# Kernel tuning notes

Measured on AMD Instinct MI355X. Metric: run time of the kernel, lower is better.

The kernel has to match this reference:

```python
import jax, jax.numpy as jnp
import numpy as np
import math

HIDDEN = 1024
HEADS = 16
HEAD_DIM = HIDDEN // HEADS
B, S = 4, 2048


def setup_inputs() -> dict:
    key = jax.random.key(0)
    ks = jax.random.split(key, 9)
    std = 1.0 / math.sqrt(HIDDEN)
    return {
        "query": jax.random.normal(ks[0], (B, S, HIDDEN), jnp.float32),
        "key": jax.random.normal(ks[1], (B, S, HIDDEN), jnp.float32),
        "value": jax.random.normal(ks[2], (B, S, HIDDEN), jnp.float32),
        "q_w": jax.random.normal(ks[3], (HIDDEN, HIDDEN), jnp.float32) * std,
        "q_b": jax.random.normal(ks[4], (HIDDEN,), jnp.float32) * 0.02,
        "k_w": jax.random.normal(ks[5], (HIDDEN, HIDDEN), jnp.float32) * std,
        "k_b": jax.random.normal(ks[6], (HIDDEN,), jnp.float32) * 0.02,
        "v_w": jax.random.normal(ks[7], (HIDDEN, HIDDEN), jnp.float32) * std,
        "v_b": jax.random.normal(ks[8], (HIDDEN,), jnp.float32) * 0.02,
    }


def _split_heads(x):
    # [B, S, H] -> [B, heads, S, head_dim]
    b, s, _ = x.shape
    return x.reshape(b, s, HEADS, HEAD_DIM).transpose(0, 2, 1, 3)


def reference(query, key, value, q_w, q_b, k_w, k_b, v_w, v_b):
    # Linear projections (torch Linear: x @ W^T + b; here weights stored as [in, out])
    q = _split_heads(query @ q_w + q_b)   # [B, h, S, d]
    k = _split_heads(key @ k_w + k_b)
    v = _split_heads(value @ v_w + v_b)
    scale = 1.0 / math.sqrt(HEAD_DIM)
    scores = jnp.einsum("bhqd,bhkd->bhqk", q, k) * scale  # [B, h, S, S]
    # NOTE: faithful to source bug — context uses raw scaled scores, NOT softmax probs.
    # (softmax is computed in the original but its result is unused for the output.)
    ctx = jnp.einsum("bhqk,bhkd->bhqd", scores, v)
    ctx = ctx.transpose(0, 2, 1, 3).reshape(query.shape[0], query.shape[1], HIDDEN)
    return ctx
```

## Files before the change

kernel.cpp:

```cpp
#include <hip/hip_runtime.h>
#include <stdint.h>

#define HIDDEN 1024
#define HEADS 16
#define HEAD_DIM 64
#define BATCH 4
#define SEQ 2048
#define ROWS (BATCH * SEQ)

typedef float f32x4 __attribute__((ext_vector_type(4)));
typedef short bf16x8 __attribute__((ext_vector_type(8)));

__device__ __forceinline__ uint16_t f32_to_bf16_rne(float f) {
    uint32_t u = __float_as_uint(f);
    uint32_t r = u + 0x7FFFu + ((u >> 16) & 1u);
    return (uint16_t)(r >> 16);
}
__device__ __forceinline__ float bf16_to_f32(uint16_t u) {
    return __uint_as_float(((uint32_t)u) << 16);
}

__global__ __launch_bounds__(256) void cvt_kernel(const float* __restrict__ Xq,
                                                  const float* __restrict__ Xk,
                                                  const float* __restrict__ Xv,
                                                  uint16_t* __restrict__ Xb) {
    int z = blockIdx.x >> 11;
    const float* X = z == 0 ? Xq : (z == 1 ? Xk : Xv);
    uint16_t* out = Xb + (size_t)z * ROWS * HIDDEN;
    size_t base = (size_t)(blockIdx.x & 2047) * 1024 + threadIdx.x;
    const float4* Xi = (const float4*)X;
    float4 f0 = Xi[base];
    float4 f1 = Xi[base + 256];
    float4 f2 = Xi[base + 512];
    float4 f3 = Xi[base + 768];
    uint2* Oi = (uint2*)out;
    uint2 p;
    p.x = (uint32_t)f32_to_bf16_rne(f0.x) | ((uint32_t)f32_to_bf16_rne(f0.y) << 16);
    p.y = (uint32_t)f32_to_bf16_rne(f0.z) | ((uint32_t)f32_to_bf16_rne(f0.w) << 16);
    Oi[base] = p;
    p.x = (uint32_t)f32_to_bf16_rne(f1.x) | ((uint32_t)f32_to_bf16_rne(f1.y) << 16);
    p.y = (uint32_t)f32_to_bf16_rne(f1.z) | ((uint32_t)f32_to_bf16_rne(f1.w) << 16);
    Oi[base + 256] = p;
    p.x = (uint32_t)f32_to_bf16_rne(f2.x) | ((uint32_t)f32_to_bf16_rne(f2.y) << 16);
    p.y = (uint32_t)f32_to_bf16_rne(f2.z) | ((uint32_t)f32_to_bf16_rne(f2.w) << 16);
    Oi[base + 512] = p;
    p.x = (uint32_t)f32_to_bf16_rne(f3.x) | ((uint32_t)f32_to_bf16_rne(f3.y) << 16);
    p.y = (uint32_t)f32_to_bf16_rne(f3.z) | ((uint32_t)f32_to_bf16_rne(f3.w) << 16);
    Oi[base + 768] = p;
}

__global__ __launch_bounds__(256) void wt_kernel(const float* __restrict__ Wk,
                                                 const float* __restrict__ Wv,
                                                 uint16_t* __restrict__ Wt) {
    const float* W = blockIdx.z == 0 ? Wk : Wv;
    uint16_t* out = Wt + (size_t)blockIdx.z * HIDDEN * HIDDEN;
    __shared__ float tile[64][65];
    int k0 = blockIdx.x * 64, n0 = blockIdx.y * 64;
    int r = threadIdx.x >> 6, c = threadIdx.x & 63;
    for (int it = 0; it < 16; ++it) {
        int rr = r + 4 * it;
        tile[rr][c] = W[(size_t)(k0 + rr) * HIDDEN + n0 + c];
    }
    __syncthreads();
    for (int it = 0; it < 16; ++it) {
        int rr = r + 4 * it;
        out[(size_t)(n0 + rr) * HIDDEN + k0 + c] = f32_to_bf16_rne(tile[c][rr]);
    }
}

__global__ __launch_bounds__(256) void proj_gemm(const uint16_t* __restrict__ Xkv,
                                                 const uint16_t* __restrict__ Wt,
                                                 const float* __restrict__ Bk,
                                                 const float* __restrict__ Bv,
                                                 uint16_t* __restrict__ KV) {
    const int z = blockIdx.z;
    const uint16_t* X = Xkv + (size_t)z * ROWS * HIDDEN;
    const uint16_t* W = Wt + (size_t)z * HIDDEN * HIDDEN;
    const float* bias = z == 0 ? Bk : Bv;
    uint16_t* out = KV + (size_t)z * ROWS * HIDDEN;

    __shared__ uint16_t slds[16384];

    const int tid = threadIdx.x;
    const int lane = tid & 63;
    const int w = tid >> 6;
    const int wm = (w >> 1) * 64;
    const int wn = (w & 1) * 64;
    const int m_lane = lane & 15;
    const int kq = lane >> 4;
    const int m0 = blockIdx.x * 128;
    const int n0 = blockIdx.y * 128;

    f32x4 acc[4][4] = {};

    for (int kb = 0; kb < HIDDEN; kb += 64) {
        for (int t = 0; t < 4; ++t) {
            int gbase = (w * 4 + t) * 64;
            int g = gbase + lane;
            int r = g >> 3;
            int c = (g & 7) ^ (r & 7);
            const uint16_t* srcA = X + (size_t)(m0 + r) * HIDDEN + kb + c * 8;
            __builtin_amdgcn_global_load_lds(
                (const __attribute__((address_space(1))) uint32_t*)srcA,
                (__attribute__((address_space(3))) uint32_t*)(&slds[gbase * 8]),
                16, 0, 0);
            const uint16_t* srcB = W + (size_t)(n0 + r) * HIDDEN + kb + c * 8;
            __builtin_amdgcn_global_load_lds(
                (const __attribute__((address_space(1))) uint32_t*)srcB,
                (__attribute__((address_space(3))) uint32_t*)(&slds[8192 + gbase * 8]),
                16, 0, 0);
        }
        __syncthreads();
        for (int ks = 0; ks < 2; ++ks) {
            int cbase = ks * 4 + kq;
            bf16x8 af[4], bfr[4];
            for (int i = 0; i < 4; ++i) {
                int r = wm + i * 16 + m_lane;
                int p = cbase ^ (r & 7);
                af[i] = *(const bf16x8*)(&slds[r * 64 + p * 8]);
            }
            for (int j = 0; j < 4; ++j) {
                int nr = wn + j * 16 + m_lane;
                int p = cbase ^ (nr & 7);
                bfr[j] = *(const bf16x8*)(&slds[8192 + nr * 64 + p * 8]);
            }
            for (int i = 0; i < 4; ++i)
                for (int j = 0; j < 4; ++j)
                    acc[i][j] = __builtin_amdgcn_mfma_f32_16x16x32_bf16(
                        af[i], bfr[j], acc[i][j], 0, 0, 0);
        }
        __syncthreads();
    }

    for (int j = 0; j < 4; ++j) {
        int col = n0 + wn + j * 16 + m_lane;
        float bj = bias[col];
        for (int i = 0; i < 4; ++i) {
            int rbase = m0 + wm + i * 16 + kq * 4;
            for (int rg = 0; rg < 4; ++rg) {
                float v = acc[i][j][rg] + bj;
                out[(size_t)(rbase + rg) * HIDDEN + col] = f32_to_bf16_rne(v);
            }
        }
    }
}

__global__ __launch_bounds__(256) void kv_kernel(const uint16_t* __restrict__ KV,
                                                 float* __restrict__ P) {
    const uint16_t* K = KV;
    const uint16_t* V = KV + (size_t)ROWS * HIDDEN;
    const int bh = blockIdx.x;
    const int sc = blockIdx.y;
    const int b = bh >> 4, h = bh & 15;
    const int tid = threadIdx.x;
    const size_t base = ((size_t)b * SEQ + sc * 256) * HIDDEN + h * 64;

    __shared__ float kk[16][64];
    __shared__ float vv[16][64];
    float acc[4][4] = {};
    const int i0 = (tid >> 4) * 4, j0 = (tid & 15) * 4;

    for (int batch = 0; batch < 16; ++batch) {
        __syncthreads();
        {
            int t = tid & 127;
            int row = t >> 3, c = t & 7;
            const uint16_t* src =
                (tid < 128 ? K : V) + base + (size_t)(batch * 16 + row) * HIDDEN + c * 8;
            float* dst = (tid < 128 ? &kk[row][c * 8] : &vv[row][c * 8]);
            bf16x8 d = *(const bf16x8*)src;
            for (int e = 0; e < 8; ++e) dst[e] = bf16_to_f32((uint16_t)d[e]);
        }
        __syncthreads();
        for (int r = 0; r < 16; ++r) {
            f32x4 ka = *(const f32x4*)(&kk[r][i0]);
            f32x4 va = *(const f32x4*)(&vv[r][j0]);
            for (int a = 0; a < 4; ++a)
                for (int bb = 0; bb < 4; ++bb)
                    acc[a][bb] += ka[a] * va[bb];
        }
    }
    float* Pp = P + ((size_t)bh * 8 + sc) * 4096;
    for (int a = 0; a < 4; ++a) {
        f32x4 row;
        for (int bb = 0; bb < 4; ++bb) row[bb] = acc[a][bb] * 0.125f;
        *(f32x4*)(&Pp[(i0 + a) * 64 + j0]) = row;
    }
}

__global__ __launch_bounds__(256) void wprime_kernel(const float* __restrict__ Wq,
                                                     const float* __restrict__ bq,
                                                     const float* __restrict__ P,
                                                     uint16_t* __restrict__ Wpt,
                                                     float* __restrict__ bp) {
    const int h = blockIdx.x;
    const int r0 = blockIdx.y * 64;
    const int b = blockIdx.z;
    const int tid = threadIdx.x;

    __shared__ float Mh[64][65];
    __shared__ float Wl[64][65];
    const float* Pp = P + ((size_t)(b * 16 + h)) * 8 * 4096;
    for (int it = 0; it < 16; ++it) {
        int e = it * 256 + tid;
        int a = e >> 6, c = e & 63;
        float s = 0.f;
        for (int sc = 0; sc < 8; ++sc) s += Pp[sc * 4096 + e];
        Mh[a][c] = s;
        Wl[a][c] = Wq[(size_t)(r0 + a) * HIDDEN + h * 64 + c];
    }
    __syncthreads();

    const int r = tid & 63;
    const int jbase = tid >> 6;
    float acc[16] = {};
    for (int i = 0; i < 64; ++i) {
        float wv = Wl[r][i];
        for (int jj = 0; jj < 16; ++jj)
            acc[jj] += wv * Mh[i][jbase + 4 * jj];
    }
    uint16_t* Wb = Wpt + (size_t)b * HIDDEN * HIDDEN;
    for (int jj = 0; jj < 16; ++jj) {
        int n = h * 64 + jbase + 4 * jj;
        Wb[(size_t)n * HIDDEN + r0 + r] = f32_to_bf16_rne(acc[jj]);
    }

    if (blockIdx.y == 0 && tid < 64) {
        int j = tid;
        float s = 0.f;
        for (int i = 0; i < 64; ++i) s += bq[h * 64 + i] * Mh[i][j];
        bp[b * HIDDEN + h * 64 + j] = s;
    }
}

__global__ __launch_bounds__(256) void final_gemm(const uint16_t* __restrict__ Xq,
                                                  const uint16_t* __restrict__ Wpt,
                                                  const float* __restrict__ bp,
                                                  float* __restrict__ out) {
    __shared__ uint16_t slds[16384];

    const int tid = threadIdx.x;
    const int lane = tid & 63;
    const int w = tid >> 6;
    const int wm = (w >> 1) * 64;
    const int wn = (w & 1) * 64;
    const int m_lane = lane & 15;
    const int kq = lane >> 4;
    const int m0 = blockIdx.x * 128;
    const int n0 = blockIdx.y * 128;
    const int batch = m0 >> 11;
    const uint16_t* W = Wpt + (size_t)batch * HIDDEN * HIDDEN;
    const float* bias = bp + batch * HIDDEN;

    f32x4 acc[4][4] = {};

    for (int kb = 0; kb < HIDDEN; kb += 64) {
        for (int t = 0; t < 4; ++t) {
            int gbase = (w * 4 + t) * 64;
            int g = gbase + lane;
            int r = g >> 3;
            int c = (g & 7) ^ (r & 7);
            const uint16_t* srcA = Xq + (size_t)(m0 + r) * HIDDEN + kb + c * 8;
            __builtin_amdgcn_global_load_lds(
                (const __attribute__((address_space(1))) uint32_t*)srcA,
                (__attribute__((address_space(3))) uint32_t*)(&slds[gbase * 8]),
                16, 0, 0);
            const uint16_t* srcB = W + (size_t)(n0 + r) * HIDDEN + kb + c * 8;
            __builtin_amdgcn_global_load_lds(
                (const __attribute__((address_space(1))) uint32_t*)srcB,
                (__attribute__((address_space(3))) uint32_t*)(&slds[8192 + gbase * 8]),
                16, 0, 0);
        }
        __syncthreads();
        for (int ks = 0; ks < 2; ++ks) {
            int cbase = ks * 4 + kq;
            bf16x8 af[4], bfr[4];
            for (int i = 0; i < 4; ++i) {
                int r = wm + i * 16 + m_lane;
                int p = cbase ^ (r & 7);
                af[i] = *(const bf16x8*)(&slds[r * 64 + p * 8]);
            }
            for (int j = 0; j < 4; ++j) {
                int nr = wn + j * 16 + m_lane;
                int p = cbase ^ (nr & 7);
                bfr[j] = *(const bf16x8*)(&slds[8192 + nr * 64 + p * 8]);
            }
            for (int i = 0; i < 4; ++i)
                for (int j = 0; j < 4; ++j)
                    acc[i][j] = __builtin_amdgcn_mfma_f32_16x16x32_bf16(
                        af[i], bfr[j], acc[i][j], 0, 0, 0);
        }
        __syncthreads();
    }

    for (int j = 0; j < 4; ++j) {
        int col = n0 + wn + j * 16 + m_lane;
        float bj = bias[col];
        for (int i = 0; i < 4; ++i) {
            int rbase = m0 + wm + i * 16 + kq * 4;
            for (int rg = 0; rg < 4; ++rg)
                out[(size_t)(rbase + rg) * HIDDEN + col] = acc[i][j][rg] + bj;
        }
    }
}

extern "C" void kernel_launch(void* const* d_in, const int* in_sizes, int n_in,
                              void* d_out, int out_size, void* d_ws, size_t ws_size,
                              hipStream_t stream) {
    const float* Xq = (const float*)d_in[0];
    const float* Xk = (const float*)d_in[1];
    const float* Xv = (const float*)d_in[2];
    const float* Wq = (const float*)d_in[3];
    const float* Bq = (const float*)d_in[4];
    const float* Wk = (const float*)d_in[5];
    const float* Bk = (const float*)d_in[6];
    const float* Wv = (const float*)d_in[7];
    const float* Bv = (const float*)d_in[8];
    float* out = (float*)d_out;

    char* ws = (char*)d_ws;
    uint16_t* Xb = (uint16_t*)ws;
    uint16_t* KV = (uint16_t*)(ws + 50331648);
    uint16_t* Wt = (uint16_t*)(ws + 83886080);
    float* P = (float*)(ws + 88080384);
    uint16_t* Wpt = (uint16_t*)(ws + 96468992);
    float* bp = (float*)(ws + 104857600);

    cvt_kernel<<<dim3(3 * 2048), 256, 0, stream>>>(Xq, Xk, Xv, Xb);
    wt_kernel<<<dim3(16, 16, 2), 256, 0, stream>>>(Wk, Wv, Wt);

    const uint16_t* Xkv = Xb + (size_t)ROWS * HIDDEN;
    proj_gemm<<<dim3(64, 8, 2), 256, 0, stream>>>(Xkv, Wt, Bk, Bv, KV);
    kv_kernel<<<dim3(64, 8), 256, 0, stream>>>(KV, P);
    wprime_kernel<<<dim3(16, 16, 4), 256, 0, stream>>>(Wq, Bq, P, Wpt, bp);
    final_gemm<<<dim3(64, 8), 256, 0, stream>>>(Xb, Wpt, bp, out);
}
```

Baseline: 272.2 us.

## Reassociate K^T V via input Gram matrix instead of projecting K and V

Instead of projecting K and V over all 8192 rows and then forming per-head K^T V, this computes the per-batch Gram matrix Xv^T Xk (1024x1024 over 2048 tokens) and then multiplies it by the weights. Bias terms are added through row sums of the inputs and small matvec kernels. This removes the large projection GEMM but adds transposed bf16 conversions, an extra 1024^3-per-batch GEMM, atomics and several small kernels. Precision changes too, because the Gram matrix is stored in bf16.

```diff
diff --git a/kernel.cpp b/kernel.cpp
--- a/kernel.cpp
+++ b/kernel.cpp
@@ -20,20 +20,15 @@
     return __uint_as_float(((uint32_t)u) << 16);
 }
 
-__global__ __launch_bounds__(256) void cvt_kernel(const float* __restrict__ Xq,
-                                                  const float* __restrict__ Xk,
-                                                  const float* __restrict__ Xv,
-                                                  uint16_t* __restrict__ Xb) {
-    int z = blockIdx.x >> 11;
-    const float* X = z == 0 ? Xq : (z == 1 ? Xk : Xv);
-    uint16_t* out = Xb + (size_t)z * ROWS * HIDDEN;
-    size_t base = (size_t)(blockIdx.x & 2047) * 1024 + threadIdx.x;
-    const float4* Xi = (const float4*)X;
+__global__ __launch_bounds__(256) void cvt_q(const float* __restrict__ Xq,
+                                             uint16_t* __restrict__ XqB) {
+    size_t base = (size_t)blockIdx.x * 1024 + threadIdx.x;
+    const float4* Xi = (const float4*)Xq;
     float4 f0 = Xi[base];
     float4 f1 = Xi[base + 256];
     float4 f2 = Xi[base + 512];
     float4 f3 = Xi[base + 768];
-    uint2* Oi = (uint2*)out;
+    uint2* Oi = (uint2*)XqB;
     uint2 p;
     p.x = (uint32_t)f32_to_bf16_rne(f0.x) | ((uint32_t)f32_to_bf16_rne(f0.y) << 16);
     p.y = (uint32_t)f32_to_bf16_rne(f0.z) | ((uint32_t)f32_to_bf16_rne(f0.w) << 16);
@@ -49,6 +44,36 @@
     Oi[base + 768] = p;
 }
 
+__global__ __launch_bounds__(256) void cvt_t(const float* __restrict__ Xk,
+                                             const float* __restrict__ Xv,
+                                             uint16_t* __restrict__ XkT,
+                                             uint16_t* __restrict__ XvT,
+                                             float* __restrict__ rk,
+                                             float* __restrict__ rv) {
+    const int z = blockIdx.z >> 2, b = blockIdx.z & 3;
+    const float* X = z ? Xv : Xk;
+    uint16_t* XT = z ? XvT : XkT;
+    float* rsum = z ? rv : rk;
+    __shared__ float tile[64][65];
+    const int s0 = blockIdx.x * 64, i0 = blockIdx.y * 64;
+    const int r = threadIdx.x >> 6, c = threadIdx.x & 63;
+    for (int it = 0; it < 16; ++it) {
+        int rr = r + 4 * it;
+        tile[rr][c] = X[(size_t)(b * SEQ + s0 + rr) * HIDDEN + i0 + c];
+    }
+    __syncthreads();
+    for (int it = 0; it < 16; ++it) {
+        int rr = r + 4 * it;
+        XT[(size_t)b * (HIDDEN * SEQ) + (size_t)(i0 + rr) * SEQ + s0 + c] =
+            f32_to_bf16_rne(tile[c][rr]);
+    }
+    if (threadIdx.x < 64) {
+        float s = 0.f;
+        for (int row = 0; row < 64; ++row) s += tile[row][threadIdx.x];
+        atomicAdd(&rsum[b * HIDDEN + i0 + threadIdx.x], s);
+    }
+}
+
 __global__ __launch_bounds__(256) void wt_kernel(const float* __restrict__ Wk,
                                                  const float* __restrict__ Wv,
                                                  uint16_t* __restrict__ Wt) {
@@ -68,16 +93,14 @@
     }
 }
 
-__global__ __launch_bounds__(256) void proj_gemm(const uint16_t* __restrict__ Xkv,
-                                                 const uint16_t* __restrict__ Wt,
-                                                 const float* __restrict__ Bk,
-                                                 const float* __restrict__ Bv,
-                                                 uint16_t* __restrict__ KV) {
-    const int z = blockIdx.z;
-    const uint16_t* X = Xkv + (size_t)z * ROWS * HIDDEN;
-    const uint16_t* W = Wt + (size_t)z * HIDDEN * HIDDEN;
-    const float* bias = z == 0 ? Bk : Bv;
-    uint16_t* out = KV + (size_t)z * ROWS * HIDDEN;
+template <bool BF16OUT>
+__global__ __launch_bounds__(256) void gemm_bt(const uint16_t* __restrict__ A,
+                                               const uint16_t* __restrict__ B,
+                                               void* __restrict__ Cv, int K,
+                                               size_t sA, size_t sB, size_t sC) {
+    const int b = blockIdx.z;
+    const uint16_t* Ab = A + sA * b;
+    const uint16_t* Bb = B + sB * b;
 
     __shared__ uint16_t slds[16384];
 
@@ -93,18 +116,18 @@
 
     f32x4 acc[4][4] = {};
 
-    for (int kb = 0; kb < HIDDEN; kb += 64) {
+    for (int kb = 0; kb < K; kb += 64) {
         for (int t = 0; t < 4; ++t) {
             int gbase = (w * 4 + t) * 64;
             int g = gbase + lane;
             int r = g >> 3;
             int c = (g & 7) ^ (r & 7);
-            const uint16_t* srcA = X + (size_t)(m0 + r) * HIDDEN + kb + c * 8;
+            const uint16_t* srcA = Ab + (size_t)(m0 + r) * K + kb + c * 8;
             __builtin_amdgcn_global_load_lds(
                 (const __attribute__((address_space(1))) uint32_t*)srcA,
                 (__attribute__((address_space(3))) uint32_t*)(&slds[gbase * 8]),
                 16, 0, 0);
-            const uint16_t* srcB = W + (size_t)(n0 + r) * HIDDEN + kb + c * 8;
+            const uint16_t* srcB = Bb + (size_t)(n0 + r) * K + kb + c * 8;
             __builtin_amdgcn_global_load_lds(
                 (const __attribute__((address_space(1))) uint32_t*)srcB,
                 (__attribute__((address_space(3))) uint32_t*)(&slds[8192 + gbase * 8]),
@@ -134,57 +157,98 @@
 
     for (int j = 0; j < 4; ++j) {
         int col = n0 + wn + j * 16 + m_lane;
-        float bj = bias[col];
         for (int i = 0; i < 4; ++i) {
             int rbase = m0 + wm + i * 16 + kq * 4;
             for (int rg = 0; rg < 4; ++rg) {
-                float v = acc[i][j][rg] + bj;
-                out[(size_t)(rbase + rg) * HIDDEN + col] = f32_to_bf16_rne(v);
-            }
-        }
-    }
-}
-
-__global__ __launch_bounds__(256) void kv_kernel(const uint16_t* __restrict__ KV,
-                                                 float* __restrict__ P) {
-    const uint16_t* K = KV;
-    const uint16_t* V = KV + (size_t)ROWS * HIDDEN;
-    const int bh = blockIdx.x;
-    const int sc = blockIdx.y;
-    const int b = bh >> 4, h = bh & 15;
+                float v = acc[i][j][rg];
+                size_t idx = sC * b + (size_t)(rbase + rg) * 1024 + col;
+                if (BF16OUT)
+                    ((uint16_t*)Cv)[idx] = f32_to_bf16_rne(v);
+                else
+                    ((float*)Cv)[idx] = v;
+            }
+        }
+    }
+}
+
+__global__ __launch_bounds__(256) void kvq_kernel(const uint16_t* __restrict__ Wkt,
+                                                  const uint16_t* __restrict__ Wvt,
+                                                  const float* __restrict__ rk,
+                                                  const float* __restrict__ rv,
+                                                  float* __restrict__ kq,
+                                                  float* __restrict__ vvv) {
+    const int b = blockIdx.y;
+    const int n = blockIdx.x * 256 + threadIdx.x;
+    float s1 = 0.f, s2 = 0.f;
+    for (int i = 0; i < HIDDEN; i += 8) {
+        bf16x8 wk8 = *(const bf16x8*)(Wkt + (size_t)n * HIDDEN + i);
+        bf16x8 wv8 = *(const bf16x8*)(Wvt + (size_t)n * HIDDEN + i);
+        for (int e = 0; e < 8; ++e) {
+            s1 += bf16_to_f32((uint16_t)wk8[e]) * rk[b * HIDDEN + i + e];
+            s2 += bf16_to_f32((uint16_t)wv8[e]) * rv[b * HIDDEN + i + e];
+        }
+    }
+    kq[b * HIDDEN + n] = s1;
+    vvv[b * HIDDEN + n] = s2;
+}
+
+__global__ __launch_bounds__(256) void m_kernel(const float* __restrict__ T32,
+                                                const uint16_t* __restrict__ Wvt,
+                                                const float* __restrict__ kq,
+                                                const float* __restrict__ vvv,
+                                                const float* __restrict__ Bk,
+                                                const float* __restrict__ Bv,
+                                                float* __restrict__ P) {
+    const int h = blockIdx.x, b = blockIdx.y, jc = blockIdx.z;
     const int tid = threadIdx.x;
-    const size_t base = ((size_t)b * SEQ + sc * 256) * HIDDEN + h * 64;
-
-    __shared__ float kk[16][64];
-    __shared__ float vv[16][64];
+    __shared__ float tt[16][64];
+    __shared__ float vl[16][64];
     float acc[4][4] = {};
-    const int i0 = (tid >> 4) * 4, j0 = (tid & 15) * 4;
-
-    for (int batch = 0; batch < 16; ++batch) {
-        __syncthreads();
-        {
-            int t = tid & 127;
-            int row = t >> 3, c = t & 7;
-            const uint16_t* src =
-                (tid < 128 ? K : V) + base + (size_t)(batch * 16 + row) * HIDDEN + c * 8;
-            float* dst = (tid < 128 ? &kk[row][c * 8] : &vv[row][c * 8]);
-            bf16x8 d = *(const bf16x8*)src;
-            for (int e = 0; e < 8; ++e) dst[e] = bf16_to_f32((uint16_t)d[e]);
+    const int p0 = (tid >> 4) * 4, q0 = (tid & 15) * 4;
+    const int jbase = jc * 256;
+
+    for (int jb = 0; jb < 16; ++jb) {
+        __syncthreads();
+        if (tid < 128) {
+            int p = tid >> 1, half = tid & 1;
+            const float* src = T32 + (size_t)b * (HIDDEN * HIDDEN) +
+                               (size_t)(h * 64 + p) * HIDDEN + jbase + jb * 16 + half * 8;
+            float4 d0 = *(const float4*)src;
+            float4 d1 = *(const float4*)(src + 4);
+            tt[half * 8 + 0][p] = d0.x; tt[half * 8 + 1][p] = d0.y;
+            tt[half * 8 + 2][p] = d0.z; tt[half * 8 + 3][p] = d0.w;
+            tt[half * 8 + 4][p] = d1.x; tt[half * 8 + 5][p] = d1.y;
+            tt[half * 8 + 6][p] = d1.z; tt[half * 8 + 7][p] = d1.w;
+        } else {
+            int t2 = tid - 128;
+            int q = t2 >> 1, half = t2 & 1;
+            bf16x8 d = *(const bf16x8*)(Wvt + (size_t)(h * 64 + q) * HIDDEN +
+                                        jbase + jb * 16 + half * 8);
+            for (int e = 0; e < 8; ++e) vl[half * 8 + e][q] = bf16_to_f32((uint16_t)d[e]);
         }
         __syncthreads();
         for (int r = 0; r < 16; ++r) {
-            f32x4 ka = *(const f32x4*)(&kk[r][i0]);
-            f32x4 va = *(const f32x4*)(&vv[r][j0]);
+            f32x4 ka = *(const f32x4*)(&tt[r][p0]);
+            f32x4 va = *(const f32x4*)(&vl[r][q0]);
             for (int a = 0; a < 4; ++a)
                 for (int bb = 0; bb < 4; ++bb)
                     acc[a][bb] += ka[a] * va[bb];
         }
     }
-    float* Pp = P + ((size_t)bh * 8 + sc) * 4096;
+
+    float* Pp = P + ((size_t)(b * 16 + h) * 4 + jc) * 4096;
     for (int a = 0; a < 4; ++a) {
         f32x4 row;
-        for (int bb = 0; bb < 4; ++bb) row[bb] = acc[a][bb] * 0.125f;
-        *(f32x4*)(&Pp[(i0 + a) * 64 + j0]) = row;
+        for (int bb = 0; bb < 4; ++bb) {
+            float v = acc[a][bb];
+            if (jc == 0) {
+                int hp = h * 64 + p0 + a, hq = h * 64 + q0 + bb;
+                v += Bk[hp] * vvv[b * HIDDEN + hq] + kq[b * HIDDEN + hp] * Bv[hq] +
+                     2048.0f * Bk[hp] * Bv[hq];
+            }
+            row[bb] = v * 0.125f;
+        }
+        *(f32x4*)(&Pp[(p0 + a) * 64 + q0]) = row;
     }
 }
 
@@ -200,12 +264,12 @@
 
     __shared__ float Mh[64][65];
     __shared__ float Wl[64][65];
-    const float* Pp = P + ((size_t)(b * 16 + h)) * 8 * 4096;
+    const float* Pp = P + (size_t)(b * 16 + h) * 4 * 4096;
     for (int it = 0; it < 16; ++it) {
         int e = it * 256 + tid;
         int a = e >> 6, c = e & 63;
         float s = 0.f;
-        for (int sc = 0; sc < 8; ++sc) s += Pp[sc * 4096 + e];
+        for (int sc = 0; sc < 4; ++sc) s += Pp[sc * 4096 + e];
         Mh[a][c] = s;
         Wl[a][c] = Wq[(size_t)(r0 + a) * HIDDEN + h * 64 + c];
     }
@@ -319,19 +383,37 @@
     float* out = (float*)d_out;
 
     char* ws = (char*)d_ws;
-    uint16_t* Xb = (uint16_t*)ws;
-    uint16_t* KV = (uint16_t*)(ws + 50331648);
-    uint16_t* Wt = (uint16_t*)(ws + 83886080);
-    float* P = (float*)(ws + 88080384);
-    uint16_t* Wpt = (uint16_t*)(ws + 96468992);
-    float* bp = (float*)(ws + 104857600);
-
-    cvt_kernel<<<dim3(3 * 2048), 256, 0, stream>>>(Xq, Xk, Xv, Xb);
+    uint16_t* XqB = (uint16_t*)ws;
+    uint16_t* XkT = (uint16_t*)(ws + 16777216);
+    uint16_t* XvT = (uint16_t*)(ws + 33554432);
+    uint16_t* Wt = (uint16_t*)(ws + 50331648);
+    uint16_t* Gt = (uint16_t*)(ws + 54525952);
+    float* T32 = (float*)(ws + 62914560);
+    float* P = (float*)(ws + 79691776);
+    uint16_t* Wpt = (uint16_t*)(ws + 83886080);
+    float* bp = (float*)(ws + 92274688);
+    float* rk = (float*)(ws + 92291072);
+    float* rv = (float*)(ws + 92307456);
+    float* kq = (float*)(ws + 92323840);
+    float* vvv = (float*)(ws + 92340224);
+
+    const uint16_t* Wkt = Wt;
+    const uint16_t* Wvt = Wt + (size_t)HIDDEN * HIDDEN;
+
+    hipMemsetAsync(ws + 92291072, 0, 32768, stream);
+
+    cvt_q<<<dim3(2048), 256, 0, stream>>>(Xq, XqB);
+    cvt_t<<<dim3(32, 16, 8), 256, 0, stream>>>(Xk, Xv, XkT, XvT, rk, rv);
     wt_kernel<<<dim3(16, 16, 2), 256, 0, stream>>>(Wk, Wv, Wt);
 
-    const uint16_t* Xkv = Xb + (size_t)ROWS * HIDDEN;
-    proj_gemm<<<dim3(64, 8, 2), 256, 0, stream>>>(Xkv, Wt, Bk, Bv, KV);
-    kv_kernel<<<dim3(64, 8), 256, 0, stream>>>(KV, P);
+    gemm_bt<true><<<dim3(8, 8, 4), 256, 0, stream>>>(
+        XvT, XkT, Gt, 2048, (size_t)HIDDEN * SEQ, (size_t)HIDDEN * SEQ,
+        (size_t)HIDDEN * HIDDEN);
+    gemm_bt<false><<<dim3(8, 8, 4), 256, 0, stream>>>(
+        Wkt, Gt, T32, 1024, 0, (size_t)HIDDEN * HIDDEN, (size_t)HIDDEN * HIDDEN);
+
+    kvq_kernel<<<dim3(4, 4), 256, 0, stream>>>(Wkt, Wvt, rk, rv, kq, vvv);
+    m_kernel<<<dim3(16, 4, 4), 256, 0, stream>>>(T32, Wvt, kq, vvv, Bk, Bv, P);
     wprime_kernel<<<dim3(16, 16, 4), 256, 0, stream>>>(Wq, Bq, P, Wpt, bp);
-    final_gemm<<<dim3(64, 8), 256, 0, stream>>>(Xb, Wpt, bp, out);
-}
+    final_gemm<<<dim3(64, 8), 256, 0, stream>>>(XqB, Wpt, bp, out);
+}
```

Result: slower. 333.7 us (+22.6%).
